# Kernel optimization log

Hardware: AMD Instinct MI355X
Metric: run time of the kernel (lower is better)

The kernel has to match this reference:

```python
import jax, jax.numpy as jnp
import numpy as np

EPS = 1e-5

def _layer_norm(x, w):
    mu = jnp.mean(x, axis=-1, keepdims=True)
    var = jnp.mean(jnp.square(x - mu), axis=-1, keepdims=True)
    return (x - mu) * jax.lax.rsqrt(var + EPS) * w

def setup_inputs() -> dict:
    key = jax.random.key(0)
    ks = jax.random.split(key, 5)
    B, T, C, H = 2, 2048, 1024, 16
    std = 0.02
    return {
        "x": jax.random.normal(ks[0], (B, T, C), dtype=jnp.float32),
        "ln1_w": jnp.ones((C,), dtype=jnp.float32),
        "w_attn": jax.random.normal(ks[1], (C, 3 * C), dtype=jnp.float32) * std,
        "w_proj": jax.random.normal(ks[2], (C, C), dtype=jnp.float32) * std,
        "ln2_w": jnp.ones((C,), dtype=jnp.float32),
        "w_fc": jax.random.normal(ks[3], (C, 4 * C), dtype=jnp.float32) * std,
        "w_cproj": jax.random.normal(ks[4], (4 * C, C), dtype=jnp.float32) * std,
    }

def reference(x, ln1_w, w_attn, w_proj, ln2_w, w_fc, w_cproj):
    B, T, C = x.shape
    H = 16
    Dh = C // H
    # --- causal self-attention on ln1(x) ---
    h = _layer_norm(x, ln1_w)
    qkv = h @ w_attn                      # [B,T,3C]
    q, k, v = jnp.split(qkv, 3, axis=-1)
    # [B,T,C] -> [B,H,T,Dh]
    q = q.reshape(B, T, H, Dh).transpose(0, 2, 1, 3)
    k = k.reshape(B, T, H, Dh).transpose(0, 2, 1, 3)
    v = v.reshape(B, T, H, Dh).transpose(0, 2, 1, 3)
    # NOTE: original scales by full embed dim C**-0.5, not head_dim**-0.5
    scores = jnp.einsum('bhqd,bhkd->bhqk', q, k) * (C ** -0.5)
    causal = jnp.tril(jnp.ones((T, T), dtype=bool))
    scores = jnp.where(causal, scores, -jnp.inf)
    probs = jax.nn.softmax(scores, axis=-1)  # dropout=0.0 (eval)
    y = jnp.einsum('bhqk,bhkd->bhqd', probs, v)
    y = y.transpose(0, 2, 1, 3).reshape(B, T, C)
    x = x + y @ w_proj
    # --- MLP on ln2(x) ---
    h = _layer_norm(x, ln2_w)
    x = x + jax.nn.relu(h @ w_fc) @ w_cproj
    return x
```

## Files before the change

### kernel.cpp

```cpp
#include <hip/hip_runtime.h>

typedef __attribute__((ext_vector_type(8))) __bf16 bf16x8;
typedef __attribute__((ext_vector_type(4))) float f32x4;
typedef __attribute__((ext_vector_type(8))) unsigned short u16x8;
typedef __attribute__((ext_vector_type(4))) unsigned short u16x4;
typedef unsigned short u16;

__device__ __forceinline__ u16 f2bf(float f) {
  return __builtin_bit_cast(u16, (__bf16)f);
}
__device__ __forceinline__ float bf2f(u16 u) {
  return __builtin_bit_cast(float, ((unsigned)u) << 16);
}

__device__ __forceinline__ f32x4 mfma16(bf16x8 a, bf16x8 b, f32x4 c) {
  return __builtin_amdgcn_mfma_f32_16x16x32_bf16(a, b, c, 0, 0, 0);
}

__device__ __forceinline__ void gl_lds16(const void* g, void* l) {
  __builtin_amdgcn_global_load_lds(
      (const __attribute__((address_space(1))) unsigned int*)g,
      (__attribute__((address_space(3))) unsigned int*)l, 16, 0, 0);
}

__device__ __forceinline__ f32x4 fmax4(f32x4 a, f32x4 b) {
  f32x4 r;
  r[0] = fmaxf(a[0], b[0]); r[1] = fmaxf(a[1], b[1]);
  r[2] = fmaxf(a[2], b[2]); r[3] = fmaxf(a[3], b[3]);
  return r;
}

__global__ __launch_bounds__(256) void convT(const float* __restrict__ in,
                                             u16* __restrict__ outT, int K, int N) {
  __shared__ float tile[64][65];
  const int t = threadIdx.x;
  const int tk = blockIdx.x * 64, tn = blockIdx.y * 64;
  const int lk = t >> 4, ln = (t & 15) * 4;
#pragma unroll
  for (int r = 0; r < 4; ++r) {
    const int k = lk + r * 16;
    const float4 v = *(const float4*)(in + (size_t)(tk + k) * N + tn + ln);
    tile[k][ln + 0] = v.x; tile[k][ln + 1] = v.y;
    tile[k][ln + 2] = v.z; tile[k][ln + 3] = v.w;
  }
  __syncthreads();
  const int sn = t >> 2, sk = (t & 3) * 4;
#pragma unroll
  for (int j = 0; j < 4; ++j) {
    const int k = sk + j * 16;
    ushort4 o;
    o.x = f2bf(tile[k + 0][sn]); o.y = f2bf(tile[k + 1][sn]);
    o.z = f2bf(tile[k + 2][sn]); o.w = f2bf(tile[k + 3][sn]);
    *(ushort4*)(outT + (size_t)(tn + sn) * K + tk + k) = o;
  }
}

__global__ __launch_bounds__(256) void ln_bf16(const float* __restrict__ x,
                                               const float* __restrict__ wgt,
                                               u16* __restrict__ out) {
  const int row = blockIdx.x, t = threadIdx.x;
  const float4 v = ((const float4*)(x + (size_t)row * 1024))[t];
  float s = v.x + v.y + v.z + v.w;
  float q = v.x * v.x + v.y * v.y + v.z * v.z + v.w * v.w;
#pragma unroll
  for (int d = 32; d; d >>= 1) { s += __shfl_xor(s, d); q += __shfl_xor(q, d); }
  __shared__ float sb[8];
  const int wv = t >> 6;
  if ((t & 63) == 0) { sb[wv] = s; sb[4 + wv] = q; }
  __syncthreads();
  s = sb[0] + sb[1] + sb[2] + sb[3];
  q = sb[4] + sb[5] + sb[6] + sb[7];
  const float mu = s * (1.f / 1024.f);
  const float rstd = rsqrtf(q * (1.f / 1024.f) - mu * mu + 1e-5f);
  const float4 w4 = ((const float4*)wgt)[t];
  ushort4 o;
  o.x = f2bf((v.x - mu) * rstd * w4.x);
  o.y = f2bf((v.y - mu) * rstd * w4.y);
  o.z = f2bf((v.z - mu) * rstd * w4.z);
  o.w = f2bf((v.w - mu) * rstd * w4.w);
  *(ushort4*)(out + (size_t)row * 1024 + t * 4) = o;
}

__global__ __launch_bounds__(256) void reduce_ln(const float* __restrict__ x,
                                                 const u16* __restrict__ p, int nseg,
                                                 const float* __restrict__ wgt,
                                                 float* __restrict__ x1,
                                                 u16* __restrict__ h2) {
  const int row = blockIdx.x, t = threadIdx.x;
  const size_t ro = (size_t)row * 1024 + t * 4;
  float4 v = *(const float4*)(x + ro);
  for (int sgm = 0; sgm < nseg; ++sgm) {
    const ushort4 u = *(const ushort4*)(p + (size_t)sgm * 4096 * 1024 + ro);
    v.x += bf2f(u.x); v.y += bf2f(u.y); v.z += bf2f(u.z); v.w += bf2f(u.w);
  }
  *(float4*)(x1 + ro) = v;
  float s = v.x + v.y + v.z + v.w;
  float q = v.x * v.x + v.y * v.y + v.z * v.z + v.w * v.w;
#pragma unroll
  for (int d = 32; d; d >>= 1) { s += __shfl_xor(s, d); q += __shfl_xor(q, d); }
  __shared__ float sb[8];
  const int wv = t >> 6;
  if ((t & 63) == 0) { sb[wv] = s; sb[4 + wv] = q; }
  __syncthreads();
  s = sb[0] + sb[1] + sb[2] + sb[3];
  q = sb[4] + sb[5] + sb[6] + sb[7];
  const float mu = s * (1.f / 1024.f);
  const float rstd = rsqrtf(q * (1.f / 1024.f) - mu * mu + 1e-5f);
  const float4 w4 = ((const float4*)wgt)[t];
  ushort4 o;
  o.x = f2bf((v.x - mu) * rstd * w4.x);
  o.y = f2bf((v.y - mu) * rstd * w4.y);
  o.z = f2bf((v.z - mu) * rstd * w4.z);
  o.w = f2bf((v.w - mu) * rstd * w4.w);
  *(ushort4*)(h2 + ro) = o;
}

__global__ __launch_bounds__(256) void reduce_out(const float* __restrict__ x1,
                                                  const u16* __restrict__ p, int nseg,
                                                  float* __restrict__ out) {
  const int i = blockIdx.x * blockDim.x + threadIdx.x;
  const size_t ro = (size_t)i * 4;
  float4 v = *(const float4*)(x1 + ro);
  for (int sgm = 0; sgm < nseg; ++sgm) {
    const ushort4 u = *(const ushort4*)(p + (size_t)sgm * 4096 * 1024 + ro);
    v.x += bf2f(u.x); v.y += bf2f(u.y); v.z += bf2f(u.z); v.w += bf2f(u.w);
  }
  *(float4*)(out + ro) = v;
}

template <int EPI>
__global__ __launch_bounds__(256) void gemm128(const u16* __restrict__ A,
                                               const u16* __restrict__ Bt,
                                               void* __restrict__ outp,
                                               int M, int N, int K) {
  __shared__ u16 As[2][4096];
  __shared__ u16 Bs[2][4096];
  const unsigned gx = gridDim.x, gy = gridDim.y, gxy = gx * gy;
  const unsigned nwg = gxy * gridDim.z;
  unsigned f = (blockIdx.z * gy + blockIdx.y) * gx + blockIdx.x;
  if ((nwg & 7u) == 0u) { const unsigned qq = nwg >> 3; f = (f & 7u) * qq + (f >> 3); }
  const int bx = f % gx, by = (f / gx) % gy, bz = f / gxy;

  const int t = threadIdx.x, w = t >> 6, l = t & 63;
  const int lr = l & 15, g = l >> 4;
  const int row0 = by * 128, col0 = bx * 128;
  const int segK = K / gridDim.z;
  const int k0 = bz * segK, kend = k0 + segK;
  const int wr = w >> 1, wc = w & 1;
  f32x4 acc[4][4] = {};

  const int sr = t >> 2;
  const int sk = (t & 3) << 3;
  const u16* Ag = A + (size_t)(row0 + sr) * K + sk;
  const u16* Bg = Bt + (size_t)(col0 + sr) * K + sk;
  const size_t rstride = (size_t)64 * K;

  auto stage = [&](int kt, int bb) {
    u16* AsW = As[bb] + w * 512;
    u16* BsW = Bs[bb] + w * 512;
    gl_lds16(Ag + kt, AsW);
    gl_lds16(Ag + kt + rstride, AsW + 2048);
    gl_lds16(Bg + kt, BsW);
    gl_lds16(Bg + kt + rstride, BsW + 2048);
  };

  stage(k0, 0);
  __syncthreads();
  int cur = 0;
  for (int kt = k0; kt < kend; kt += 32) {
    if (kt + 32 < kend) stage(kt + 32, cur ^ 1);
    bf16x8 af[4], bfr[4];
#pragma unroll
    for (int m = 0; m < 4; ++m)
      af[m] = *(const bf16x8*)(As[cur] + (wr * 64 + m * 16 + lr) * 32 + g * 8);
#pragma unroll
    for (int n = 0; n < 4; ++n)
      bfr[n] = *(const bf16x8*)(Bs[cur] + (wc * 64 + n * 16 + lr) * 32 + g * 8);
#pragma unroll
    for (int m = 0; m < 4; ++m)
#pragma unroll
      for (int n = 0; n < 4; ++n) acc[m][n] = mfma16(af[m], bfr[n], acc[m][n]);
    __syncthreads();
    cur ^= 1;
  }

  const size_t segoff = (size_t)bz * M * N;
#pragma unroll
  for (int m = 0; m < 4; ++m)
#pragma unroll
    for (int n = 0; n < 4; ++n)
#pragma unroll
      for (int r = 0; r < 4; ++r) {
        const int row = row0 + wr * 64 + m * 16 + g * 4 + r;
        const int col = col0 + wc * 64 + n * 16 + lr;
        const size_t idx = (size_t)row * N + col;
        const float v = acc[m][n][r];
        if constexpr (EPI == 0) ((u16*)outp)[idx] = f2bf(v);
        else if constexpr (EPI == 2) ((u16*)outp)[idx] = f2bf(fmaxf(v, 0.f));
        else ((u16*)outp)[segoff + idx] = f2bf(v);
      }
}

__global__ __launch_bounds__(256) void attn_fwd(const u16* __restrict__ qkvb,
                                                u16* __restrict__ y) {
  __shared__ u16 Ks[2][4096];
  __shared__ u16 Vt[64 * 80];
  __shared__ u16 Pb[4][16 * 72];
  const int t = threadIdx.x, w = t >> 6, l = t & 63;
  const int lr = l & 15, g = l >> 4;
  const unsigned f = blockIdx.y * gridDim.x + blockIdx.x;
  const int xcd = f & 7, j = f >> 3;
  const int bh = xcd + 8 * (j & 3);
  const int qt = 31 - (j >> 2);
  const int b = bh >> 4, h = bh & 15;
  const size_t base = (size_t)b * 2048 * 3072;
  const u16* Kg = qkvb + base + 1024 + h * 64;
  const u16* Vg = qkvb + base + 2048 + h * 64;
  u16* Pw = &Pb[w][0];
  const int vkv = t & 63;
  const int vd0 = (t >> 6) * 16;
  const float SCL = 0.0450842200277855f;

  auto stageK = [&](int kv0, int bb) {
#pragma unroll
    for (int r = 0; r < 2; ++r) {
      const int dl = (r * 256 + t) * 16;
      const int row = dl >> 7;
      const int srcb = (dl & 127) ^ ((row & 7) << 4);
      gl_lds16(Kg + (size_t)(kv0 + row) * 3072 + (srcb >> 1),
               (char*)Ks[bb] + r * 4096 + w * 1024);
    }
  };

  const int q0 = qt * 64, q0w = q0 + w * 16, nt = qt + 1;
  const u16* Qp = qkvb + base + (size_t)(q0w + lr) * 3072 + h * 64;
  const bf16x8 qf0 = *(const bf16x8*)(Qp + g * 8);
  const bf16x8 qf1 = *(const bf16x8*)(Qp + 32 + g * 8);
  f32x4 o[4] = {};
  float m1 = -1e30f, s1 = 0.f;

  stageK(0, 0);
  u16x8 v0 = *(const u16x8*)(Vg + (size_t)vkv * 3072 + vd0);
  u16x8 v1 = *(const u16x8*)(Vg + (size_t)vkv * 3072 + vd0 + 8);
#pragma unroll
  for (int jj = 0; jj < 8; ++jj) {
    Vt[(vd0 + jj) * 80 + vkv] = v0[jj];
    Vt[(vd0 + 8 + jj) * 80 + vkv] = v1[jj];
  }
  __syncthreads();

  int ct = 0;
  for (int tt = 0; tt < nt; ++tt) {
    const int kv0 = tt * 64;
    const bool more = (tt + 1 < nt);
    if (more) {
      stageK(kv0 + 64, ct ^ 1);
      v0 = *(const u16x8*)(Vg + (size_t)(kv0 + 64 + vkv) * 3072 + vd0);
      v1 = *(const u16x8*)(Vg + (size_t)(kv0 + 64 + vkv) * 3072 + vd0 + 8);
    }

    const u16* Kbuf = Ks[ct];
    f32x4 s4[4];
#pragma unroll
    for (int i = 0; i < 4; ++i) {
      const int row = i * 16 + lr;
      const int sw = (row & 7) << 4;
      const bf16x8 k0 = *(const bf16x8*)(Kbuf + row * 64 + (((g * 16) ^ sw) >> 1));
      const bf16x8 k1 = *(const bf16x8*)(Kbuf + row * 64 + (((64 + g * 16) ^ sw) >> 1));
      f32x4 z = {0.f, 0.f, 0.f, 0.f};
      z = mfma16(k0, qf0, z);
      z = mfma16(k1, qf1, z);
      s4[i] = z * SCL;
    }
    if (kv0 + 64 > q0w) {
#pragma unroll
      for (int i = 0; i < 4; ++i)
#pragma unroll
        for (int r = 0; r < 4; ++r)
          if (kv0 + i * 16 + g * 4 + r > q0w + lr) s4[i][r] = -1e30f;
    }
    const f32x4 mm = fmax4(fmax4(s4[0], s4[1]), fmax4(s4[2], s4[3]));
    float mx = fmaxf(fmaxf(mm[0], mm[1]), fmaxf(mm[2], mm[3]));
    mx = fmaxf(mx, __shfl_xor(mx, 16));
    mx = fmaxf(mx, __shfl_xor(mx, 32));
    if (!__all(mx <= m1 + 8.f)) {
      const float mn = fmaxf(m1, mx);
      const float sc = exp2f(m1 - mn);
      m1 = mn;
      s1 *= sc;
      float scr[4];
#pragma unroll
      for (int r = 0; r < 4; ++r) scr[r] = __shfl(sc, g * 4 + r);
#pragma unroll
      for (int n = 0; n < 4; ++n)
#pragma unroll
        for (int r = 0; r < 4; ++r) o[n][r] *= scr[r];
    }
    float ps = 0.f;
#pragma unroll
    for (int i = 0; i < 4; ++i) {
      u16x4 pk;
#pragma unroll
      for (int r = 0; r < 4; ++r) {
        const float p = exp2f(s4[i][r] - m1);
        ps += p;
        pk[r] = f2bf(p);
      }
      *(u16x4*)(Pw + lr * 72 + i * 16 + g * 4) = pk;
    }
    s1 += ps;
#pragma unroll
    for (int s = 0; s < 2; ++s) {
      const bf16x8 pa = *(const bf16x8*)(Pw + lr * 72 + s * 32 + g * 8);
#pragma unroll
      for (int n = 0; n < 4; ++n) {
        const bf16x8 vf = *(const bf16x8*)(&Vt[(n * 16 + lr) * 80 + s * 32 + g * 8]);
        o[n] = mfma16(pa, vf, o[n]);
      }
    }
    __syncthreads();
    if (more) {
#pragma unroll
      for (int jj = 0; jj < 8; ++jj) {
        Vt[(vd0 + jj) * 80 + vkv] = v0[jj];
        Vt[(vd0 + 8 + jj) * 80 + vkv] = v1[jj];
      }
    }
    __syncthreads();
    ct ^= 1;
  }

  float den = s1;
  den += __shfl_xor(den, 16);
  den += __shfl_xor(den, 32);
  const float iv = 1.f / den;
  float ivr[4];
#pragma unroll
  for (int r = 0; r < 4; ++r) ivr[r] = __shfl(iv, g * 4 + r);
#pragma unroll
  for (int n = 0; n < 4; ++n)
#pragma unroll
    for (int r = 0; r < 4; ++r) {
      const int row = q0w + g * 4 + r;
      const int col = h * 64 + n * 16 + lr;
      y[(size_t)(b * 2048 + row) * 1024 + col] = f2bf(o[n][r] * ivr[r]);
    }
}

extern "C" void kernel_launch(void* const* d_in, const int* in_sizes, int n_in,
                              void* d_out, int out_size, void* d_ws, size_t ws_size,
                              hipStream_t stream) {
  const float* x      = (const float*)d_in[0];
  const float* ln1w   = (const float*)d_in[1];
  const float* wattn  = (const float*)d_in[2];
  const float* wproj  = (const float*)d_in[3];
  const float* ln2w   = (const float*)d_in[4];
  const float* wfc    = (const float*)d_in[5];
  const float* wcproj = (const float*)d_in[6];
  float* out = (float*)d_out;
  char* ws = (char*)d_ws;
  const size_t MB = 1024 * 1024;
  u16* qkvb    = (u16*)(ws + 0);
  u16* cprojP  = (u16*)(ws + 0);
  u16* h1      = (u16*)(ws + 24 * MB);
  u16* yb      = (u16*)(ws + 24 * MB);
  u16* projP   = (u16*)(ws + 32 * MB);
  float* x1    = (float*)(ws + 48 * MB);
  u16* h2      = (u16*)(ws + 64 * MB);
  u16* hf      = (u16*)(ws + 72 * MB);
  u16* wattnT  = (u16*)(ws + 104 * MB);
  u16* wprojT  = (u16*)(ws + 110 * MB);
  u16* wcprojT = (u16*)(ws + 104 * MB);
  u16* wfcT    = (u16*)(ws + 112 * MB);

  convT<<<dim3(16, 48), 256, 0, stream>>>(wattn, wattnT, 1024, 3072);
  convT<<<dim3(16, 16), 256, 0, stream>>>(wproj, wprojT, 1024, 1024);
  convT<<<dim3(16, 64), 256, 0, stream>>>(wfc, wfcT, 1024, 4096);

  ln_bf16<<<4096, 256, 0, stream>>>(x, ln1w, h1);
  gemm128<0><<<dim3(24, 32, 1), 256, 0, stream>>>(h1, wattnT, qkvb, 4096, 3072, 1024);
  attn_fwd<<<dim3(32, 32), 256, 0, stream>>>(qkvb, yb);
  gemm128<4><<<dim3(8, 32, 2), 256, 0, stream>>>(yb, wprojT, projP, 4096, 1024, 1024);
  convT<<<dim3(64, 16), 256, 0, stream>>>(wcproj, wcprojT, 4096, 1024);
  reduce_ln<<<4096, 256, 0, stream>>>(x, projP, 2, ln2w, x1, h2);
  gemm128<2><<<dim3(32, 32, 1), 256, 0, stream>>>(h2, wfcT, hf, 4096, 4096, 1024);
  gemm128<4><<<dim3(8, 32, 4), 256, 0, stream>>>(hf, wcprojT, cprojP, 4096, 1024, 4096);
  reduce_out<<<4096, 256, 0, stream>>>(x1, cprojP, 4, out);
}
```

Baseline: 258.7 us.

## Process 128 query rows per attention block and double-buffer transposed V

```diff
diff --git a/kernel.cpp b/kernel.cpp
--- a/kernel.cpp
+++ b/kernel.cpp
@@ -204,14 +204,14 @@
 __global__ __launch_bounds__(256) void attn_fwd(const u16* __restrict__ qkvb,
                                                 u16* __restrict__ y) {
   __shared__ u16 Ks[2][4096];
-  __shared__ u16 Vt[64 * 80];
-  __shared__ u16 Pb[4][16 * 72];
+  __shared__ u16 Vt[2][64 * 80];
+  __shared__ u16 Pb[4][32 * 72];
   const int t = threadIdx.x, w = t >> 6, l = t & 63;
   const int lr = l & 15, g = l >> 4;
   const unsigned f = blockIdx.y * gridDim.x + blockIdx.x;
   const int xcd = f & 7, j = f >> 3;
   const int bh = xcd + 8 * (j & 3);
-  const int qt = 31 - (j >> 2);
+  const int qp = 15 - (j >> 2);
   const int b = bh >> 4, h = bh & 15;
   const size_t base = (size_t)b * 2048 * 3072;
   const u16* Kg = qkvb + base + 1024 + h * 64;
@@ -232,20 +232,25 @@
     }
   };
 
-  const int q0 = qt * 64, q0w = q0 + w * 16, nt = qt + 1;
+  const int q0w = qp * 128 + w * 32;
+  const int nt = 2 * qp + 2;
   const u16* Qp = qkvb + base + (size_t)(q0w + lr) * 3072 + h * 64;
-  const bf16x8 qf0 = *(const bf16x8*)(Qp + g * 8);
-  const bf16x8 qf1 = *(const bf16x8*)(Qp + 32 + g * 8);
-  f32x4 o[4] = {};
-  float m1 = -1e30f, s1 = 0.f;
+  bf16x8 qf[2][2];
+#pragma unroll
+  for (int qh = 0; qh < 2; ++qh) {
+    qf[qh][0] = *(const bf16x8*)(Qp + qh * 16 * 3072 + g * 8);
+    qf[qh][1] = *(const bf16x8*)(Qp + qh * 16 * 3072 + 32 + g * 8);
+  }
+  f32x4 o[2][4] = {};
+  float m1[2] = {-1e30f, -1e30f}, s1[2] = {0.f, 0.f};
 
   stageK(0, 0);
   u16x8 v0 = *(const u16x8*)(Vg + (size_t)vkv * 3072 + vd0);
   u16x8 v1 = *(const u16x8*)(Vg + (size_t)vkv * 3072 + vd0 + 8);
 #pragma unroll
   for (int jj = 0; jj < 8; ++jj) {
-    Vt[(vd0 + jj) * 80 + vkv] = v0[jj];
-    Vt[(vd0 + 8 + jj) * 80 + vkv] = v1[jj];
+    Vt[0][(vd0 + jj) * 80 + vkv] = v0[jj];
+    Vt[0][(vd0 + 8 + jj) * 80 + vkv] = v1[jj];
   }
   __syncthreads();
 
@@ -260,91 +265,104 @@
     }
 
     const u16* Kbuf = Ks[ct];
-    f32x4 s4[4];
+    bf16x8 kf[4][2];
 #pragma unroll
     for (int i = 0; i < 4; ++i) {
       const int row = i * 16 + lr;
       const int sw = (row & 7) << 4;
-      const bf16x8 k0 = *(const bf16x8*)(Kbuf + row * 64 + (((g * 16) ^ sw) >> 1));
-      const bf16x8 k1 = *(const bf16x8*)(Kbuf + row * 64 + (((64 + g * 16) ^ sw) >> 1));
-      f32x4 z = {0.f, 0.f, 0.f, 0.f};
-      z = mfma16(k0, qf0, z);
-      z = mfma16(k1, qf1, z);
-      s4[i] = z * SCL;
-    }
-    if (kv0 + 64 > q0w) {
-#pragma unroll
-      for (int i = 0; i < 4; ++i)
-#pragma unroll
-        for (int r = 0; r < 4; ++r)
-          if (kv0 + i * 16 + g * 4 + r > q0w + lr) s4[i][r] = -1e30f;
-    }
-    const f32x4 mm = fmax4(fmax4(s4[0], s4[1]), fmax4(s4[2], s4[3]));
-    float mx = fmaxf(fmaxf(mm[0], mm[1]), fmaxf(mm[2], mm[3]));
-    mx = fmaxf(mx, __shfl_xor(mx, 16));
-    mx = fmaxf(mx, __shfl_xor(mx, 32));
-    if (!__all(mx <= m1 + 8.f)) {
-      const float mn = fmaxf(m1, mx);
-      const float sc = exp2f(m1 - mn);
-      m1 = mn;
-      s1 *= sc;
-      float scr[4];
-#pragma unroll
-      for (int r = 0; r < 4; ++r) scr[r] = __shfl(sc, g * 4 + r);
-#pragma unroll
-      for (int n = 0; n < 4; ++n)
-#pragma unroll
-        for (int r = 0; r < 4; ++r) o[n][r] *= scr[r];
-    }
-    float ps = 0.f;
-#pragma unroll
-    for (int i = 0; i < 4; ++i) {
-      u16x4 pk;
-#pragma unroll
-      for (int r = 0; r < 4; ++r) {
-        const float p = exp2f(s4[i][r] - m1);
-        ps += p;
-        pk[r] = f2bf(p);
-      }
-      *(u16x4*)(Pw + lr * 72 + i * 16 + g * 4) = pk;
-    }
-    s1 += ps;
+      kf[i][0] = *(const bf16x8*)(Kbuf + row * 64 + (((g * 16) ^ sw) >> 1));
+      kf[i][1] = *(const bf16x8*)(Kbuf + row * 64 + (((64 + g * 16) ^ sw) >> 1));
+    }
+#pragma unroll
+    for (int qh = 0; qh < 2; ++qh) {
+      f32x4 s4[4];
+#pragma unroll
+      for (int i = 0; i < 4; ++i) {
+        f32x4 z = {0.f, 0.f, 0.f, 0.f};
+        z = mfma16(kf[i][0], qf[qh][0], z);
+        z = mfma16(kf[i][1], qf[qh][1], z);
+        s4[i] = z * SCL;
+      }
+      const int qrow = q0w + qh * 16 + lr;
+      if (kv0 + 64 > qrow) {
+#pragma unroll
+        for (int i = 0; i < 4; ++i)
+#pragma unroll
+          for (int r = 0; r < 4; ++r)
+            if (kv0 + i * 16 + g * 4 + r > qrow) s4[i][r] = -1e30f;
+      }
+      const f32x4 mm = fmax4(fmax4(s4[0], s4[1]), fmax4(s4[2], s4[3]));
+      float mx = fmaxf(fmaxf(mm[0], mm[1]), fmaxf(mm[2], mm[3]));
+      mx = fmaxf(mx, __shfl_xor(mx, 16));
+      mx = fmaxf(mx, __shfl_xor(mx, 32));
+      if (!__all(mx <= m1[qh] + 8.f)) {
+        const float mn = fmaxf(m1[qh], mx);
+        const float sc = exp2f(m1[qh] - mn);
+        m1[qh] = mn;
+        s1[qh] *= sc;
+        float scr[4];
+#pragma unroll
+        for (int r = 0; r < 4; ++r) scr[r] = __shfl(sc, g * 4 + r);
+#pragma unroll
+        for (int n = 0; n < 4; ++n)
+#pragma unroll
+          for (int r = 0; r < 4; ++r) o[qh][n][r] *= scr[r];
+      }
+      float ps = 0.f;
+#pragma unroll
+      for (int i = 0; i < 4; ++i) {
+        u16x4 pk;
+#pragma unroll
+        for (int r = 0; r < 4; ++r) {
+          const float p = exp2f(s4[i][r] - m1[qh]);
+          ps += p;
+          pk[r] = f2bf(p);
+        }
+        *(u16x4*)(Pw + (qh * 16 + lr) * 72 + i * 16 + g * 4) = pk;
+      }
+      s1[qh] += ps;
+    }
 #pragma unroll
     for (int s = 0; s < 2; ++s) {
-      const bf16x8 pa = *(const bf16x8*)(Pw + lr * 72 + s * 32 + g * 8);
+      const bf16x8 pa0 = *(const bf16x8*)(Pw + lr * 72 + s * 32 + g * 8);
+      const bf16x8 pa1 = *(const bf16x8*)(Pw + (16 + lr) * 72 + s * 32 + g * 8);
 #pragma unroll
       for (int n = 0; n < 4; ++n) {
-        const bf16x8 vf = *(const bf16x8*)(&Vt[(n * 16 + lr) * 80 + s * 32 + g * 8]);
-        o[n] = mfma16(pa, vf, o[n]);
-      }
-    }
-    __syncthreads();
+        const bf16x8 vf =
+            *(const bf16x8*)(&Vt[ct][(n * 16 + lr) * 80 + s * 32 + g * 8]);
+        o[0][n] = mfma16(pa0, vf, o[0][n]);
+        o[1][n] = mfma16(pa1, vf, o[1][n]);
+      }
+    }
     if (more) {
 #pragma unroll
       for (int jj = 0; jj < 8; ++jj) {
-        Vt[(vd0 + jj) * 80 + vkv] = v0[jj];
-        Vt[(vd0 + 8 + jj) * 80 + vkv] = v1[jj];
+        Vt[ct ^ 1][(vd0 + jj) * 80 + vkv] = v0[jj];
+        Vt[ct ^ 1][(vd0 + 8 + jj) * 80 + vkv] = v1[jj];
       }
     }
     __syncthreads();
     ct ^= 1;
   }
 
-  float den = s1;
-  den += __shfl_xor(den, 16);
-  den += __shfl_xor(den, 32);
-  const float iv = 1.f / den;
-  float ivr[4];
-#pragma unroll
-  for (int r = 0; r < 4; ++r) ivr[r] = __shfl(iv, g * 4 + r);
-#pragma unroll
-  for (int n = 0; n < 4; ++n)
-#pragma unroll
-    for (int r = 0; r < 4; ++r) {
-      const int row = q0w + g * 4 + r;
-      const int col = h * 64 + n * 16 + lr;
-      y[(size_t)(b * 2048 + row) * 1024 + col] = f2bf(o[n][r] * ivr[r]);
-    }
+#pragma unroll
+  for (int qh = 0; qh < 2; ++qh) {
+    float den = s1[qh];
+    den += __shfl_xor(den, 16);
+    den += __shfl_xor(den, 32);
+    const float iv = 1.f / den;
+    float ivr[4];
+#pragma unroll
+    for (int r = 0; r < 4; ++r) ivr[r] = __shfl(iv, g * 4 + r);
+#pragma unroll
+    for (int n = 0; n < 4; ++n)
+#pragma unroll
+      for (int r = 0; r < 4; ++r) {
+        const int row = q0w + qh * 16 + g * 4 + r;
+        const int col = h * 64 + n * 16 + lr;
+        y[(size_t)(b * 2048 + row) * 1024 + col] = f2bf(o[qh][n][r] * ivr[r]);
+      }
+  }
 }
 
 extern "C" void kernel_launch(void* const* d_in, const int* in_sizes, int n_in,
@@ -379,7 +397,7 @@
 
   ln_bf16<<<4096, 256, 0, stream>>>(x, ln1w, h1);
   gemm128<0><<<dim3(24, 32, 1), 256, 0, stream>>>(h1, wattnT, qkvb, 4096, 3072, 1024);
-  attn_fwd<<<dim3(32, 32), 256, 0, stream>>>(qkvb, yb);
+  attn_fwd<<<dim3(16, 32), 256, 0, stream>>>(qkvb, yb);
   gemm128<4><<<dim3(8, 32, 2), 256, 0, stream>>>(yb, wprojT, projP, 4096, 1024, 1024);
   convT<<<dim3(64, 16), 256, 0, stream>>>(wcproj, wcprojT, 4096, 1024);
   reduce_ln<<<4096, 256, 0, stream>>>(x, projP, 2, ln2w, x1, h2);
```

Measured after the change: 275.0 us. +6.3%, slower.

## Pre-transpose V in a separate kernel and async-stage it into double-buffered LDS

Applied to the files above, without the earlier changes.

```diff
diff --git a/kernel.cpp b/kernel.cpp
--- a/kernel.cpp
+++ b/kernel.cpp
@@ -52,6 +52,36 @@
     o.x = f2bf(tile[k + 0][sn]); o.y = f2bf(tile[k + 1][sn]);
     o.z = f2bf(tile[k + 2][sn]); o.w = f2bf(tile[k + 3][sn]);
     *(ushort4*)(outT + (size_t)(tn + sn) * K + tk + k) = o;
+  }
+}
+
+__global__ __launch_bounds__(256) void vtrans(const u16* __restrict__ qkvb,
+                                              u16* __restrict__ vT) {
+  __shared__ u16 tile[64][72];
+  const int t = threadIdx.x;
+  const int tt0 = blockIdx.x * 64;
+  const int bh = blockIdx.y;
+  const int b = bh >> 4, h = bh & 15;
+  const u16* src = qkvb + (size_t)(b * 2048 + tt0) * 3072 + 2048 + h * 64;
+  {
+    const int tl = t >> 2, d0 = (t & 3) * 16;
+    const u16x8 a0 = *(const u16x8*)(src + (size_t)tl * 3072 + d0);
+    const u16x8 a1 = *(const u16x8*)(src + (size_t)tl * 3072 + d0 + 8);
+    *(u16x8*)(&tile[tl][d0]) = a0;
+    *(u16x8*)(&tile[tl][d0 + 8]) = a1;
+  }
+  __syncthreads();
+  {
+    const int dh = t >> 2, t0 = (t & 3) * 16;
+    u16x8 o0, o1;
+#pragma unroll
+    for (int jj = 0; jj < 8; ++jj) {
+      o0[jj] = tile[t0 + jj][dh];
+      o1[jj] = tile[t0 + 8 + jj][dh];
+    }
+    u16* dst = vT + ((size_t)bh * 64 + dh) * 2048 + tt0 + t0;
+    *(u16x8*)dst = o0;
+    *(u16x8*)(dst + 8) = o1;
   }
 }
 
@@ -202,9 +232,10 @@
 }
 
 __global__ __launch_bounds__(256) void attn_fwd(const u16* __restrict__ qkvb,
+                                                const u16* __restrict__ vT,
                                                 u16* __restrict__ y) {
   __shared__ u16 Ks[2][4096];
-  __shared__ u16 Vt[64 * 80];
+  __shared__ u16 Vs[2][4096];
   __shared__ u16 Pb[4][16 * 72];
   const int t = threadIdx.x, w = t >> 6, l = t & 63;
   const int lr = l & 15, g = l >> 4;
@@ -215,10 +246,8 @@
   const int b = bh >> 4, h = bh & 15;
   const size_t base = (size_t)b * 2048 * 3072;
   const u16* Kg = qkvb + base + 1024 + h * 64;
-  const u16* Vg = qkvb + base + 2048 + h * 64;
+  const u16* Vg = vT + (size_t)bh * 64 * 2048;
   u16* Pw = &Pb[w][0];
-  const int vkv = t & 63;
-  const int vd0 = (t >> 6) * 16;
   const float SCL = 0.0450842200277855f;
 
   auto stageK = [&](int kv0, int bb) {
@@ -231,8 +260,18 @@
                (char*)Ks[bb] + r * 4096 + w * 1024);
     }
   };
-
-  const int q0 = qt * 64, q0w = q0 + w * 16, nt = qt + 1;
+  auto stageV = [&](int kv0, int bb) {
+#pragma unroll
+    for (int r = 0; r < 2; ++r) {
+      const int dl = (r * 256 + t) * 16;
+      const int dh = dl >> 7;
+      const int srcb = (dl & 127) ^ ((dh & 7) << 4);
+      gl_lds16(Vg + (size_t)dh * 2048 + kv0 + (srcb >> 1),
+               (char*)Vs[bb] + r * 4096 + w * 1024);
+    }
+  };
+
+  const int q0w = qt * 64 + w * 16, nt = qt + 1;
   const u16* Qp = qkvb + base + (size_t)(q0w + lr) * 3072 + h * 64;
   const bf16x8 qf0 = *(const bf16x8*)(Qp + g * 8);
   const bf16x8 qf1 = *(const bf16x8*)(Qp + 32 + g * 8);
@@ -240,26 +279,19 @@
   float m1 = -1e30f, s1 = 0.f;
 
   stageK(0, 0);
-  u16x8 v0 = *(const u16x8*)(Vg + (size_t)vkv * 3072 + vd0);
-  u16x8 v1 = *(const u16x8*)(Vg + (size_t)vkv * 3072 + vd0 + 8);
-#pragma unroll
-  for (int jj = 0; jj < 8; ++jj) {
-    Vt[(vd0 + jj) * 80 + vkv] = v0[jj];
-    Vt[(vd0 + 8 + jj) * 80 + vkv] = v1[jj];
-  }
+  stageV(0, 0);
   __syncthreads();
 
   int ct = 0;
   for (int tt = 0; tt < nt; ++tt) {
     const int kv0 = tt * 64;
-    const bool more = (tt + 1 < nt);
-    if (more) {
+    if (tt + 1 < nt) {
       stageK(kv0 + 64, ct ^ 1);
-      v0 = *(const u16x8*)(Vg + (size_t)(kv0 + 64 + vkv) * 3072 + vd0);
-      v1 = *(const u16x8*)(Vg + (size_t)(kv0 + 64 + vkv) * 3072 + vd0 + 8);
+      stageV(kv0 + 64, ct ^ 1);
     }
 
     const u16* Kbuf = Ks[ct];
+    const u16* Vbuf = Vs[ct];
     f32x4 s4[4];
 #pragma unroll
     for (int i = 0; i < 4; ++i) {
@@ -314,16 +346,10 @@
       const bf16x8 pa = *(const bf16x8*)(Pw + lr * 72 + s * 32 + g * 8);
 #pragma unroll
       for (int n = 0; n < 4; ++n) {
-        const bf16x8 vf = *(const bf16x8*)(&Vt[(n * 16 + lr) * 80 + s * 32 + g * 8]);
+        const int dh = n * 16 + lr;
+        const bf16x8 vf = *(const bf16x8*)(
+            Vbuf + dh * 64 + (((s * 64 + g * 16) ^ ((dh & 7) << 4)) >> 1));
         o[n] = mfma16(pa, vf, o[n]);
-      }
-    }
-    __syncthreads();
-    if (more) {
-#pragma unroll
-      for (int jj = 0; jj < 8; ++jj) {
-        Vt[(vd0 + jj) * 80 + vkv] = v0[jj];
-        Vt[(vd0 + 8 + jj) * 80 + vkv] = v1[jj];
       }
     }
     __syncthreads();
@@ -367,6 +393,7 @@
   u16* projP   = (u16*)(ws + 32 * MB);
   float* x1    = (float*)(ws + 48 * MB);
   u16* h2      = (u16*)(ws + 64 * MB);
+  u16* vT      = (u16*)(ws + 72 * MB);
   u16* hf      = (u16*)(ws + 72 * MB);
   u16* wattnT  = (u16*)(ws + 104 * MB);
   u16* wprojT  = (u16*)(ws + 110 * MB);
@@ -379,7 +406,8 @@
 
   ln_bf16<<<4096, 256, 0, stream>>>(x, ln1w, h1);
   gemm128<0><<<dim3(24, 32, 1), 256, 0, stream>>>(h1, wattnT, qkvb, 4096, 3072, 1024);
-  attn_fwd<<<dim3(32, 32), 256, 0, stream>>>(qkvb, yb);
+  vtrans<<<dim3(32, 32), 256, 0, stream>>>(qkvb, vT);
+  attn_fwd<<<dim3(32, 32), 256, 0, stream>>>(qkvb, vT, yb);
   gemm128<4><<<dim3(8, 32, 2), 256, 0, stream>>>(yb, wprojT, projP, 4096, 1024, 1024);
   convT<<<dim3(64, 16), 256, 0, stream>>>(wcproj, wcprojT, 4096, 1024);
   reduce_ln<<<4096, 256, 0, stream>>>(x, projP, 2, ln2w, x1, h2);
```

Result: faster. 252.7 us (-2.3%).
